# Kernel tuning notes

Hardware: AMD Instinct MI355X
Metric: run time of the kernel (lower is better)

The kernel has to match this reference:

```python
import jax, jax.numpy as jnp
import numpy as np

EMB = 768
HEADS = 8
B, N = 8, 1024

def _ln(x, g, b, eps=1e-5):
    mu = jnp.mean(x, axis=-1, keepdims=True)
    var = jnp.mean(jnp.square(x - mu), axis=-1, keepdims=True)
    return (x - mu) * jax.lax.rsqrt(var + eps) * g + b

def setup_inputs() -> dict:
    key = jax.random.key(0)
    ks = jax.random.split(key, 8)
    s_in = 0.02
    return {
        "x": jax.random.normal(ks[0], (B, N, EMB), jnp.float32),
        "w_qkvr": jax.random.normal(ks[1], (EMB, 4 * EMB), jnp.float32) * s_in,
        "b_qkvr": jnp.zeros((4 * EMB,), jnp.float32),
        "w_proj": jax.random.normal(ks[2], (EMB, EMB), jnp.float32) * s_in,
        "b_proj": jnp.zeros((EMB,), jnp.float32),
        "ln1_g": jnp.ones((EMB,), jnp.float32),
        "ln1_b": jnp.zeros((EMB,), jnp.float32),
        "w_ff1": jax.random.normal(ks[3], (EMB, 4 * EMB), jnp.float32) * s_in,
        "b_ff1": jnp.zeros((4 * EMB,), jnp.float32),
        "w_ff2": jax.random.normal(ks[4], (4 * EMB, EMB), jnp.float32) * s_in,
        "b_ff2": jnp.zeros((EMB,), jnp.float32),
        "ln2_g": jnp.ones((EMB,), jnp.float32),
        "ln2_b": jnp.zeros((EMB,), jnp.float32),
    }

def reference(x, w_qkvr, b_qkvr, w_proj, b_proj, ln1_g, ln1_b,
              w_ff1, b_ff1, w_ff2, b_ff2, ln2_g, ln2_b):
    b, n, e = x.shape
    h = HEADS
    d = e // h
    # fused QKV+R projection; einops '(h d qkvr)' => qkvr is the INNERMOST factor
    qkvr = (x @ w_qkvr + b_qkvr).reshape(b, n, h, d, 4)
    qkvr = jnp.transpose(qkvr, (4, 0, 2, 1, 3))  # [4, b, h, n, d]
    q, k, v, r = qkvr[0], qkvr[1], qkvr[2], qkvr[3]
    energy = jnp.einsum('bhqd,bhkd->bhqk', q, k)
    # quirk: softmax of UNSCALED logits, then divide by sqrt(emb_size) AFTER
    att = jax.nn.softmax(energy, axis=-1) / jnp.sqrt(jnp.float32(e))
    out = jnp.einsum('bhqk,bhkd->bhqd', att, v)
    out = out * r  # elementwise r-gate
    out = jnp.transpose(out, (0, 2, 1, 3)).reshape(b, n, e)
    out = out @ w_proj + b_proj
    x1 = _ln(out + x, ln1_g, ln1_b)  # residual then post-LayerNorm
    ff = jax.nn.gelu(x1 @ w_ff1 + b_ff1, approximate=False) @ w_ff2 + b_ff2
    return _ln(ff + x1, ln2_g, ln2_b)
```

## Files before the change

kernel.cpp:

```cpp
#include <hip/hip_runtime.h>
#include <math.h>


typedef __bf16 bf16_t;
typedef __bf16 bf16x4 __attribute__((ext_vector_type(4)));
typedef __bf16 bf16x8 __attribute__((ext_vector_type(8)));
typedef float f32x4 __attribute__((ext_vector_type(4)));

#define EMB   768
#define HEADS 8
#define DHEAD 96
#define BATCH 8
#define SEQ   1024
#define ROWS  (BATCH * SEQ)

__device__ __forceinline__ void load16_lds(const bf16_t* g, bf16_t* l) {
    __builtin_amdgcn_global_load_lds(
        (__attribute__((address_space(1))) unsigned int*)g,
        (__attribute__((address_space(3))) unsigned int*)l,
        16, 0, 0);
}


__global__ void cvt_bf16_kernel(const float* __restrict__ in, bf16_t* __restrict__ out, int n) {
    int stride = gridDim.x * blockDim.x;
    for (int i = blockIdx.x * blockDim.x + threadIdx.x; i < n; i += stride)
        out[i] = (bf16_t)in[i];
}

__global__ void transpose_cvt_kernel(const float* __restrict__ in, bf16_t* __restrict__ out,
                                     int K, int N) {
    __shared__ float t[32][33];
    int n0 = blockIdx.x * 32, k0 = blockIdx.y * 32;
    int tx = threadIdx.x, ty0 = threadIdx.y;
#pragma unroll
    for (int i = 0; i < 4; i++) {
        int ty = ty0 + 8 * i;
        t[ty][tx] = in[(size_t)(k0 + ty) * N + n0 + tx];
    }
    __syncthreads();
#pragma unroll
    for (int i = 0; i < 4; i++) {
        int ty = ty0 + 8 * i;
        out[(size_t)(n0 + ty) * K + k0 + tx] = (bf16_t)t[tx][ty];
    }
}

__global__ void qkvr_transpose_kernel(const float* __restrict__ in, bf16_t* __restrict__ out) {
    __shared__ float t[32][33];
    int n0 = blockIdx.x * 32, k0 = blockIdx.y * 32;
    int tx = threadIdx.x, ty0 = threadIdx.y;
    const int which = n0 / 768, hd0 = n0 % 768;
#pragma unroll
    for (int i = 0; i < 4; i++) {
        int ty = ty0 + 8 * i;
        t[ty][tx] = in[(size_t)(k0 + ty) * 3072 + (hd0 + tx) * 4 + which];
    }
    __syncthreads();
#pragma unroll
    for (int i = 0; i < 4; i++) {
        int ty = ty0 + 8 * i;
        out[(size_t)(n0 + ty) * 768 + k0 + tx] = (bf16_t)t[tx][ty];
    }
}


enum { EPI_QKVR = 0, EPI_PROJ = 1, EPI_GELU = 2, EPI_FF2 = 3 };

template <int EPI, int KDIM>
__global__ __launch_bounds__(256) void gemm_kernel(
    const bf16_t* __restrict__ A,
    const bf16_t* __restrict__ BT,
    const float* __restrict__ bias,
    bf16_t* __restrict__ qo, bf16_t* __restrict__ ko,
    bf16_t* __restrict__ vTo, bf16_t* __restrict__ ro,
    const float* __restrict__ resid,
    float* __restrict__ outf,
    bf16_t* __restrict__ outb)
{
    __shared__ __align__(16) bf16_t As[128 * 64];
    __shared__ __align__(16) bf16_t Bs[128 * 64];

    const int tid  = threadIdx.x;
    const int wave = tid >> 6, lane = tid & 63;
    const int quad = lane >> 4, col16 = lane & 15;
    const int id = blockIdx.x;
    const int bx = id >> 6;
    const int by = ((id & 7) << 3) | ((id >> 3) & 7);
    const int m0 = by * 128, n0 = bx * 128;
    const int wrow = (wave >> 1) * 64, wcol = (wave & 1) * 64;

    f32x4 acc[4][4] = {};

    size_t ga[4], gb[4];
#pragma unroll
    for (int i = 0; i < 4; i++) {
        const int u = tid + 256 * i;
        const int rr = u >> 3, j = (u & 7) ^ (rr & 7);
        ga[i] = (size_t)(m0 + rr) * KDIM + j * 8;
        gb[i] = (size_t)(n0 + rr) * KDIM + j * 8;
    }

    for (int kk = 0; kk < KDIM / 64; kk++) {
        const int k0 = kk * 64;
        __syncthreads();
#pragma unroll
        for (int i = 0; i < 4; i++) {
            load16_lds(A + ga[i] + k0, As + (tid + 256 * i) * 8);
            load16_lds(BT + gb[i] + k0, Bs + (tid + 256 * i) * 8);
        }
        __syncthreads();
#pragma unroll
        for (int kc = 0; kc < 2; kc++) {
            bf16x8 af[4], bfr[4];
#pragma unroll
            for (int t = 0; t < 4; t++) {
                const int R = wrow + t * 16 + col16;
                af[t] = *reinterpret_cast<const bf16x8*>(As + R * 64 + (((kc * 4 + quad) ^ (R & 7)) * 8));
            }
#pragma unroll
            for (int t = 0; t < 4; t++) {
                const int R = wcol + t * 16 + col16;
                bfr[t] = *reinterpret_cast<const bf16x8*>(Bs + R * 64 + (((kc * 4 + quad) ^ (R & 7)) * 8));
            }
#pragma unroll
            for (int tr = 0; tr < 4; tr++)
#pragma unroll
                for (int tc = 0; tc < 4; tc++)
                    acc[tr][tc] = __builtin_amdgcn_mfma_f32_16x16x32_bf16(af[tr], bfr[tc], acc[tr][tc], 0, 0, 0);
        }
    }

    if (EPI == EPI_QKVR) {
        const int whichb = bx / 6;
        if (whichb == 2) {
#pragma unroll
            for (int tr = 0; tr < 4; tr++) {
#pragma unroll
                for (int tc = 0; tc < 4; tc++) {
                    const int hd   = (bx % 6) * 128 + wcol + tc * 16 + col16;
                    const int head = hd / DHEAD, dd = hd % DHEAD;
                    const float bv = bias[hd * 4 + 2];
                    const int row0 = m0 + wrow + tr * 16 + quad * 4;
                    const int b = row0 >> 10, nn0 = row0 & 1023;
                    bf16x4 w;
#pragma unroll
                    for (int rg = 0; rg < 4; rg++) w[rg] = (bf16_t)(acc[tr][tc][rg] + bv);
                    *reinterpret_cast<bf16x4*>(
                        vTo + ((size_t)(b * HEADS + head) * DHEAD + dd) * SEQ + nn0) = w;
                }
            }
        } else {
            bf16_t* dst = (whichb == 0) ? qo : (whichb == 1) ? ko : ro;
#pragma unroll
            for (int tr = 0; tr < 4; tr++) {
#pragma unroll
                for (int tc = 0; tc < 4; tc++) {
                    const int hd   = (bx % 6) * 128 + wcol + tc * 16 + col16;
                    const int head = hd / DHEAD, dd = hd % DHEAD;
                    const float bv = bias[hd * 4 + whichb];
#pragma unroll
                    for (int rg = 0; rg < 4; rg++) {
                        const int row = m0 + wrow + tr * 16 + quad * 4 + rg;
                        const int b = row >> 10, nn = row & 1023;
                        dst[((size_t)(b * HEADS + head) * SEQ + nn) * DHEAD + dd] =
                            (bf16_t)(acc[tr][tc][rg] + bv);
                    }
                }
            }
        }
    } else {
#pragma unroll
        for (int tr = 0; tr < 4; tr++) {
#pragma unroll
            for (int tc = 0; tc < 4; tc++) {
#pragma unroll
                for (int rg = 0; rg < 4; rg++) {
                    const int row  = m0 + wrow + tr * 16 + quad * 4 + rg;
                    const int colg = n0 + wcol + tc * 16 + col16;
                    float v = acc[tr][tc][rg] + bias[colg];
                    if (EPI == EPI_PROJ || EPI == EPI_FF2) {
                        outf[(size_t)row * EMB + colg] = v + resid[(size_t)row * EMB + colg];
                    } else {
                        const float z = 1.5957691216057308f * v * (1.0f + 0.044715f * v * v);
                        const float g = v / (1.0f + __expf(-z));
                        outb[(size_t)row * 3072 + colg] = (bf16_t)g;
                    }
                }
            }
        }
    }
}


__global__ __launch_bounds__(256) void attn_kernel(
    const bf16_t* __restrict__ q, const bf16_t* __restrict__ k,
    const bf16_t* __restrict__ vT, const bf16_t* __restrict__ r,
    bf16_t* __restrict__ attn_out)
{
    __shared__ __align__(16) bf16_t Ks[64 * 96];
    __shared__ __align__(16) bf16_t Vs[96 * 64];
    __shared__ __align__(16) bf16_t P[4][16 * 72];

    const int tid = threadIdx.x, wave = tid >> 6, lane = tid & 63;
    const int quad = lane >> 4, col = lane & 15;
    const int bh = blockIdx.x & 63, qb = blockIdx.x >> 6;
    const int n0 = qb * 64 + wave * 16;
    const bf16_t* qp = q  + (size_t)bh * SEQ * DHEAD;
    const bf16_t* kb = k  + (size_t)bh * SEQ * DHEAD;
    const bf16_t* vb = vT + (size_t)bh * DHEAD * SEQ;
    bf16_t* Pw = P[wave];

    bf16x8 qf[3];
#pragma unroll
    for (int ks = 0; ks < 3; ks++)
        qf[ks] = *reinterpret_cast<const bf16x8*>(qp + (size_t)(n0 + col) * DHEAD + ks * 32 + quad * 8);

    const int u0 = tid, u1 = tid + 256, u2 = tid + 512;
    const int vf0 = u0 >> 3, vp0 = (u0 & 7) ^ (vf0 & 7);
    const int vf1 = u1 >> 3, vp1 = (u1 & 7) ^ (vf1 & 7);
    const int vf2 = u2 >> 3, vp2 = (u2 & 7) ^ (vf2 & 7);

    f32x4 O[6] = {};
    float lsum = 0.f;

    for (int ch = 0; ch < SEQ / 64; ch++) {
        const int kc0 = ch * 64;
        __syncthreads();
        const bf16_t* ksrc = kb + (size_t)kc0 * DHEAD;
        load16_lds(ksrc + u0 * 8, Ks + u0 * 8);
        load16_lds(ksrc + u1 * 8, Ks + u1 * 8);
        load16_lds(ksrc + u2 * 8, Ks + u2 * 8);
        load16_lds(vb + (size_t)vf0 * SEQ + kc0 + vp0 * 8, Vs + u0 * 8);
        load16_lds(vb + (size_t)vf1 * SEQ + kc0 + vp1 * 8, Vs + u1 * 8);
        load16_lds(vb + (size_t)vf2 * SEQ + kc0 + vp2 * 8, Vs + u2 * 8);
        __syncthreads();

        f32x4 s[4] = {};
#pragma unroll
        for (int ks = 0; ks < 3; ks++) {
#pragma unroll
            for (int h = 0; h < 4; h++) {
                bf16x8 kf = *reinterpret_cast<const bf16x8*>(Ks + (h * 16 + col) * DHEAD + ks * 32 + quad * 8);
                s[h] = __builtin_amdgcn_mfma_f32_16x16x32_bf16(kf, qf[ks], s[h], 0, 0, 0);
            }
        }
#pragma unroll
        for (int h = 0; h < 4; h++) {
            bf16x4 w;
#pragma unroll
            for (int rg = 0; rg < 4; rg++) {
                const float e = __expf(s[h][rg]);
                lsum += e;
                w[rg] = (bf16_t)e;
            }
            *reinterpret_cast<bf16x4*>(Pw + col * 72 + h * 16 + quad * 4) = w;
        }
        bf16x8 af0 = *reinterpret_cast<const bf16x8*>(Pw + col * 72 + quad * 8);
        bf16x8 af1 = *reinterpret_cast<const bf16x8*>(Pw + col * 72 + 32 + quad * 8);
#pragma unroll
        for (int tc = 0; tc < 6; tc++) {
            const int feat = tc * 16 + col;
            bf16x8 bv0 = *reinterpret_cast<const bf16x8*>(Vs + feat * 64 + ((quad)     ^ (col & 7)) * 8);
            bf16x8 bv1 = *reinterpret_cast<const bf16x8*>(Vs + feat * 64 + ((4 + quad) ^ (col & 7)) * 8);
            O[tc] = __builtin_amdgcn_mfma_f32_16x16x32_bf16(af0, bv0, O[tc], 0, 0, 0);
            O[tc] = __builtin_amdgcn_mfma_f32_16x16x32_bf16(af1, bv1, O[tc], 0, 0, 0);
        }
    }

    lsum += __shfl_xor(lsum, 16);
    lsum += __shfl_xor(lsum, 32);

    const float inv_sqrt_emb = 0.036084391824351615f;
    const int b = bh >> 3, h = bh & 7;
#pragma unroll
    for (int rg = 0; rg < 4; rg++) {
        const int nrow = quad * 4 + rg;
        const float lr = __shfl(lsum, nrow);
        const float scale = inv_sqrt_emb / lr;
        const int n = n0 + nrow;
#pragma unroll
        for (int tc = 0; tc < 6; tc++) {
            const int feat = tc * 16 + col;
            const float rv = (float)r[((size_t)bh * SEQ + n) * DHEAD + feat];
            attn_out[((size_t)(b * SEQ + n)) * EMB + h * DHEAD + feat] = (bf16_t)(O[tc][rg] * scale * rv);
        }
    }
}


__global__ __launch_bounds__(256) void ln_kernel(
    const float* __restrict__ in, const float* __restrict__ g, const float* __restrict__ b,
    float* __restrict__ y, bf16_t* __restrict__ yb)
{
    const int row = blockIdx.x * 4 + (threadIdx.x >> 6);
    const int lane = threadIdx.x & 63;
    const float* rp = in + (size_t)row * EMB;
    float v[12];
    float sum = 0.f;
#pragma unroll
    for (int i = 0; i < 12; i++) { v[i] = rp[lane + i * 64]; sum += v[i]; }
#pragma unroll
    for (int off = 32; off; off >>= 1) sum += __shfl_xor(sum, off);
    const float mean = sum * (1.0f / 768.0f);
    float s2 = 0.f;
#pragma unroll
    for (int i = 0; i < 12; i++) { float d = v[i] - mean; s2 += d * d; }
#pragma unroll
    for (int off = 32; off; off >>= 1) s2 += __shfl_xor(s2, off);
    const float inv = rsqrtf(s2 * (1.0f / 768.0f) + 1e-5f);
#pragma unroll
    for (int i = 0; i < 12; i++) {
        const int c = lane + i * 64;
        const float o = (v[i] - mean) * inv * g[c] + b[c];
        y[(size_t)row * EMB + c] = o;
        if (yb) yb[(size_t)row * EMB + c] = (bf16_t)o;
    }
}


extern "C" void kernel_launch(void* const* d_in, const int* in_sizes, int n_in,
                              void* d_out, int out_size, void* d_ws, size_t ws_size,
                              hipStream_t stream)
{
    const float* x      = (const float*)d_in[0];
    const float* w_qkvr = (const float*)d_in[1];
    const float* b_qkvr = (const float*)d_in[2];
    const float* w_proj = (const float*)d_in[3];
    const float* b_proj = (const float*)d_in[4];
    const float* ln1_g  = (const float*)d_in[5];
    const float* ln1_b  = (const float*)d_in[6];
    const float* w_ff1  = (const float*)d_in[7];
    const float* b_ff1  = (const float*)d_in[8];
    const float* w_ff2  = (const float*)d_in[9];
    const float* b_ff2  = (const float*)d_in[10];
    const float* ln2_g  = (const float*)d_in[11];
    const float* ln2_b  = (const float*)d_in[12];
    float* out = (float*)d_out;

    char* ws = (char*)d_ws;
    size_t off = 0;
    auto alloc = [&](size_t bytes) {
        char* p = ws + off;
        off += (bytes + 255) & ~(size_t)255;
        return (void*)p;
    };
    const size_t ACT = (size_t)ROWS * EMB;
    bf16_t* xb      = (bf16_t*)alloc(ACT * 2);
    bf16_t* wqkvrT  = (bf16_t*)alloc((size_t)3072 * 768 * 2);
    bf16_t* wprojT  = (bf16_t*)alloc((size_t)768 * 768 * 2);
    bf16_t* wff1T   = (bf16_t*)alloc((size_t)3072 * 768 * 2);
    bf16_t* wff2T   = (bf16_t*)alloc((size_t)768 * 3072 * 2);
    bf16_t* qbuf    = (bf16_t*)alloc(ACT * 2);
    bf16_t* kbuf    = (bf16_t*)alloc(ACT * 2);
    bf16_t* vTbuf   = (bf16_t*)alloc(ACT * 2);
    bf16_t* rbuf    = (bf16_t*)alloc(ACT * 2);
    bf16_t* attn_o  = (bf16_t*)alloc(ACT * 2);
    float*  x1f     = (float*)alloc(ACT * 4);
    bf16_t* x1b     = (bf16_t*)alloc(ACT * 2);
    bf16_t* ff1     = (bf16_t*)alloc((size_t)ROWS * 3072 * 2);
    float*  res     = out;

    dim3 tb32(32, 8);

    cvt_bf16_kernel<<<2048, 256, 0, stream>>>(x, xb, (int)ACT);
    qkvr_transpose_kernel<<<dim3(3072 / 32, 768 / 32), tb32, 0, stream>>>(w_qkvr, wqkvrT);
    transpose_cvt_kernel<<<dim3(768 / 32, 768 / 32), tb32, 0, stream>>>(w_proj, wprojT, 768, 768);
    transpose_cvt_kernel<<<dim3(3072 / 32, 768 / 32), tb32, 0, stream>>>(w_ff1, wff1T, 768, 3072);
    transpose_cvt_kernel<<<dim3(768 / 32, 3072 / 32), tb32, 0, stream>>>(w_ff2, wff2T, 3072, 768);

    gemm_kernel<EPI_QKVR, 768><<<24 * 64, 256, 0, stream>>>(
        xb, wqkvrT, b_qkvr, qbuf, kbuf, vTbuf, rbuf, nullptr, nullptr, nullptr);

    attn_kernel<<<dim3(SEQ / 64 * BATCH * HEADS), 256, 0, stream>>>(qbuf, kbuf, vTbuf, rbuf, attn_o);

    gemm_kernel<EPI_PROJ, 768><<<6 * 64, 256, 0, stream>>>(
        attn_o, wprojT, b_proj, nullptr, nullptr, nullptr, nullptr, x, res, nullptr);
    ln_kernel<<<2048, 256, 0, stream>>>(res, ln1_g, ln1_b, x1f, x1b);

    gemm_kernel<EPI_GELU, 768><<<24 * 64, 256, 0, stream>>>(
        x1b, wff1T, b_ff1, nullptr, nullptr, nullptr, nullptr, nullptr, nullptr, ff1);

    gemm_kernel<EPI_FF2, 3072><<<6 * 64, 256, 0, stream>>>(
        ff1, wff2T, b_ff2, nullptr, nullptr, nullptr, nullptr, x1f, res, nullptr);
    ln_kernel<<<2048, 256, 0, stream>>>(res, ln2_g, ln2_b, out, nullptr);

    (void)in_sizes; (void)n_in; (void)out_size; (void)ws_size;
}
```

Baseline: 388.8 us.

## Rewrite GEMMs as 8-wave 256x128 tiles with triple-buffered async LDS prefetch

Replaces the 4-wave 128x128 GEMM with an 8-wave, 512-thread kernel that computes 256x128 output tiles. The K loop now uses three LDS buffers, prefetching two K-tiles ahead with split staging, vmcnt waits and raw barriers, plus s_setprio around the MFMA block. Block IDs are remapped across XCDs for locality. The aim is to hide global-load latency behind MFMA work and halve B reloads per output, at the cost of more LDS (144KB per block) and fewer blocks for the small-N GEMMs.

Result: no change. 381.7 us (-1.8%).

```diff
diff --git a/kernel.cpp b/kernel.cpp
--- a/kernel.cpp
+++ b/kernel.cpp
@@ -67,8 +67,8 @@
 
 enum { EPI_QKVR = 0, EPI_PROJ = 1, EPI_GELU = 2, EPI_FF2 = 3 };
 
-template <int EPI, int KDIM>
-__global__ __launch_bounds__(256) void gemm_kernel(
+template <int EPI, int KDIM, int NBX>
+__global__ __launch_bounds__(512, 2) void gemm8p_kernel(
     const bf16_t* __restrict__ A,
     const bf16_t* __restrict__ BT,
     const float* __restrict__ bias,
@@ -78,58 +78,106 @@
     float* __restrict__ outf,
     bf16_t* __restrict__ outb)
 {
-    __shared__ __align__(16) bf16_t As[128 * 64];
-    __shared__ __align__(16) bf16_t Bs[128 * 64];
+    constexpr int NKT  = KDIM / 64;
+    constexpr int BUFE = 24576;
+
+    __shared__ __align__(16) bf16_t lds[3 * BUFE];
 
     const int tid  = threadIdx.x;
     const int wave = tid >> 6, lane = tid & 63;
     const int quad = lane >> 4, col16 = lane & 15;
-    const int id = blockIdx.x;
-    const int bx = id >> 6;
-    const int by = ((id & 7) << 3) | ((id >> 3) & 7);
-    const int m0 = by * 128, n0 = bx * 128;
-    const int wrow = (wave >> 1) * 64, wcol = (wave & 1) * 64;
+    const int wm = wave >> 1, wn = wave & 1;
+
+    const int cpx  = gridDim.x >> 3;
+    const int id   = blockIdx.x;
+    const int wgid = (id & 7) * cpx + (id >> 3);
+    const int bx = wgid % NBX, by = wgid / NBX;
+    const int m0 = by * 256, n0 = bx * 128;
+
+    size_t gA[4]; int lA[4];
+    size_t gB[2]; int lB[2];
+#pragma unroll
+    for (int i = 0; i < 4; i++) {
+        const int u = tid + 512 * i;
+        const int r = u >> 3, j = (u & 7) ^ (r & 7);
+        gA[i] = (size_t)(m0 + r) * KDIM + j * 8;
+        lA[i] = u * 8;
+    }
+#pragma unroll
+    for (int i = 0; i < 2; i++) {
+        const int u = tid + 512 * i;
+        const int r = u >> 3, j = (u & 7) ^ (r & 7);
+        gB[i] = (size_t)(n0 + r) * KDIM + j * 8;
+        lB[i] = 16384 + u * 8;
+    }
+
+#define STAGE_H0(g_, buf_) do { \
+        const int k0_ = (g_) * 64; \
+        load16_lds(A  + gA[0] + k0_, lds + (buf_) * BUFE + lA[0]); \
+        load16_lds(A  + gA[1] + k0_, lds + (buf_) * BUFE + lA[1]); \
+        load16_lds(BT + gB[0] + k0_, lds + (buf_) * BUFE + lB[0]); \
+    } while (0)
+#define STAGE_H1(g_, buf_) do { \
+        const int k0_ = (g_) * 64; \
+        load16_lds(A  + gA[2] + k0_, lds + (buf_) * BUFE + lA[2]); \
+        load16_lds(A  + gA[3] + k0_, lds + (buf_) * BUFE + lA[3]); \
+        load16_lds(BT + gB[1] + k0_, lds + (buf_) * BUFE + lB[1]); \
+    } while (0)
+
+    STAGE_H0(0, 0); STAGE_H1(0, 0);
+    STAGE_H0(1, 1); STAGE_H1(1, 1);
+    asm volatile("s_waitcnt vmcnt(6)" ::: "memory");
+    __builtin_amdgcn_s_barrier();
 
     f32x4 acc[4][4] = {};
 
-    size_t ga[4], gb[4];
-#pragma unroll
-    for (int i = 0; i < 4; i++) {
-        const int u = tid + 256 * i;
-        const int rr = u >> 3, j = (u & 7) ^ (rr & 7);
-        ga[i] = (size_t)(m0 + rr) * KDIM + j * 8;
-        gb[i] = (size_t)(n0 + rr) * KDIM + j * 8;
-    }
-
-    for (int kk = 0; kk < KDIM / 64; kk++) {
-        const int k0 = kk * 64;
-        __syncthreads();
-#pragma unroll
-        for (int i = 0; i < 4; i++) {
-            load16_lds(A + ga[i] + k0, As + (tid + 256 * i) * 8);
-            load16_lds(BT + gb[i] + k0, Bs + (tid + 256 * i) * 8);
-        }
-        __syncthreads();
+#pragma unroll 3
+    for (int g = 0; g < NKT; g++) {
+        const int buf  = g % 3;
+        const int sbuf = (g + 2) % 3;
+        const bf16_t* Ab = lds + buf * BUFE;
+        const bf16_t* Bb = Ab + 16384;
+        const bool do_stage = (g + 2 < NKT);
 #pragma unroll
         for (int kc = 0; kc < 2; kc++) {
             bf16x8 af[4], bfr[4];
 #pragma unroll
             for (int t = 0; t < 4; t++) {
-                const int R = wrow + t * 16 + col16;
-                af[t] = *reinterpret_cast<const bf16x8*>(As + R * 64 + (((kc * 4 + quad) ^ (R & 7)) * 8));
+                const int R = wm * 64 + t * 16 + col16;
+                af[t] = *reinterpret_cast<const bf16x8*>(
+                    Ab + R * 64 + (((kc * 4 + quad) ^ (R & 7)) * 8));
             }
 #pragma unroll
             for (int t = 0; t < 4; t++) {
-                const int R = wcol + t * 16 + col16;
-                bfr[t] = *reinterpret_cast<const bf16x8*>(Bs + R * 64 + (((kc * 4 + quad) ^ (R & 7)) * 8));
-            }
+                const int S = wn * 64 + t * 16 + col16;
+                bfr[t] = *reinterpret_cast<const bf16x8*>(
+                    Bb + S * 64 + (((kc * 4 + quad) ^ (S & 7)) * 8));
+            }
+            if (kc == 0) {
+                if (do_stage) STAGE_H0(g + 2, sbuf);
+            } else {
+                if (do_stage) {
+                    STAGE_H1(g + 2, sbuf);
+                    asm volatile("s_waitcnt vmcnt(6)" ::: "memory");
+                } else if (g + 2 == NKT) {
+                    asm volatile("s_waitcnt vmcnt(0)" ::: "memory");
+                }
+            }
+            __builtin_amdgcn_s_barrier();
+            __builtin_amdgcn_s_setprio(1);
 #pragma unroll
             for (int tr = 0; tr < 4; tr++)
 #pragma unroll
                 for (int tc = 0; tc < 4; tc++)
-                    acc[tr][tc] = __builtin_amdgcn_mfma_f32_16x16x32_bf16(af[tr], bfr[tc], acc[tr][tc], 0, 0, 0);
-        }
-    }
+                    acc[tr][tc] = __builtin_amdgcn_mfma_f32_16x16x32_bf16(
+                        af[tr], bfr[tc], acc[tr][tc], 0, 0, 0);
+            __builtin_amdgcn_s_setprio(0);
+            __builtin_amdgcn_sched_barrier(0);
+            __builtin_amdgcn_s_barrier();
+        }
+    }
+#undef STAGE_H0
+#undef STAGE_H1
 
     if (EPI == EPI_QKVR) {
         const int whichb = bx / 6;
@@ -138,10 +186,10 @@
             for (int tr = 0; tr < 4; tr++) {
 #pragma unroll
                 for (int tc = 0; tc < 4; tc++) {
-                    const int hd   = (bx % 6) * 128 + wcol + tc * 16 + col16;
+                    const int hd   = (bx % 6) * 128 + wn * 64 + tc * 16 + col16;
                     const int head = hd / DHEAD, dd = hd % DHEAD;
                     const float bv = bias[hd * 4 + 2];
-                    const int row0 = m0 + wrow + tr * 16 + quad * 4;
+                    const int row0 = m0 + wm * 64 + tr * 16 + quad * 4;
                     const int b = row0 >> 10, nn0 = row0 & 1023;
                     bf16x4 w;
 #pragma unroll
@@ -156,12 +204,12 @@
             for (int tr = 0; tr < 4; tr++) {
 #pragma unroll
                 for (int tc = 0; tc < 4; tc++) {
-                    const int hd   = (bx % 6) * 128 + wcol + tc * 16 + col16;
+                    const int hd   = (bx % 6) * 128 + wn * 64 + tc * 16 + col16;
                     const int head = hd / DHEAD, dd = hd % DHEAD;
                     const float bv = bias[hd * 4 + whichb];
 #pragma unroll
                     for (int rg = 0; rg < 4; rg++) {
-                        const int row = m0 + wrow + tr * 16 + quad * 4 + rg;
+                        const int row = m0 + wm * 64 + tr * 16 + quad * 4 + rg;
                         const int b = row >> 10, nn = row & 1023;
                         dst[((size_t)(b * HEADS + head) * SEQ + nn) * DHEAD + dd] =
                             (bf16_t)(acc[tr][tc][rg] + bv);
@@ -176,8 +224,8 @@
             for (int tc = 0; tc < 4; tc++) {
 #pragma unroll
                 for (int rg = 0; rg < 4; rg++) {
-                    const int row  = m0 + wrow + tr * 16 + quad * 4 + rg;
-                    const int colg = n0 + wcol + tc * 16 + col16;
+                    const int row  = m0 + wm * 64 + tr * 16 + quad * 4 + rg;
+                    const int colg = n0 + wn * 64 + tc * 16 + col16;
                     float v = acc[tr][tc][rg] + bias[colg];
                     if (EPI == EPI_PROJ || EPI == EPI_FF2) {
                         outf[(size_t)row * EMB + colg] = v + resid[(size_t)row * EMB + colg];
@@ -369,19 +417,19 @@
     transpose_cvt_kernel<<<dim3(3072 / 32, 768 / 32), tb32, 0, stream>>>(w_ff1, wff1T, 768, 3072);
     transpose_cvt_kernel<<<dim3(768 / 32, 3072 / 32), tb32, 0, stream>>>(w_ff2, wff2T, 3072, 768);
 
-    gemm_kernel<EPI_QKVR, 768><<<24 * 64, 256, 0, stream>>>(
+    gemm8p_kernel<EPI_QKVR, 768, 24><<<768, 512, 0, stream>>>(
         xb, wqkvrT, b_qkvr, qbuf, kbuf, vTbuf, rbuf, nullptr, nullptr, nullptr);
 
     attn_kernel<<<dim3(SEQ / 64 * BATCH * HEADS), 256, 0, stream>>>(qbuf, kbuf, vTbuf, rbuf, attn_o);
 
-    gemm_kernel<EPI_PROJ, 768><<<6 * 64, 256, 0, stream>>>(
+    gemm8p_kernel<EPI_PROJ, 768, 6><<<192, 512, 0, stream>>>(
         attn_o, wprojT, b_proj, nullptr, nullptr, nullptr, nullptr, x, res, nullptr);
     ln_kernel<<<2048, 256, 0, stream>>>(res, ln1_g, ln1_b, x1f, x1b);
 
-    gemm_kernel<EPI_GELU, 768><<<24 * 64, 256, 0, stream>>>(
+    gemm8p_kernel<EPI_GELU, 768, 24><<<768, 512, 0, stream>>>(
         x1b, wff1T, b_ff1, nullptr, nullptr, nullptr, nullptr, nullptr, nullptr, ff1);
 
-    gemm_kernel<EPI_FF2, 3072><<<6 * 64, 256, 0, stream>>>(
+    gemm8p_kernel<EPI_FF2, 3072, 6><<<192, 512, 0, stream>>>(
         ff1, wff2T, b_ff2, nullptr, nullptr, nullptr, nullptr, x1f, res, nullptr);
     ln_kernel<<<2048, 256, 0, stream>>>(res, ln2_g, ln2_b, out, nullptr);
 
```

## Replace 128x128 GEMM with 256x256 double-buffered 8-wave kernel and split-K FF2

Applied to the files above, without the earlier changes.

Swaps every GEMM for a 256x256-tile, 512-thread kernel. It double-buffers its LDS and issues loads asynchronously a quarter-tile ahead, with explicit vmcnt waits, barriers and raised priority around the MFMA blocks. The FF2 GEMM is split along K into two halves: the second half writes raw partial sums into the reused q buffer, and the second LayerNorm adds them in. Larger tiles and overlapped loads aim to raise operand reuse and MFMA utilisation. The trade-offs are fewer workgroups for the proj GEMM (96 blocks), heavy register pressure, and an extra fp32 partial buffer to write and read.

After: 423.7 us. +9.0%, slower.

```diff
diff --git a/kernel.cpp b/kernel.cpp
--- a/kernel.cpp
+++ b/kernel.cpp
@@ -67,8 +67,81 @@
 
 enum { EPI_QKVR = 0, EPI_PROJ = 1, EPI_GELU = 2, EPI_FF2 = 3 };
 
-template <int EPI, int KDIM>
-__global__ __launch_bounds__(256) void gemm_kernel(
+#define VMW6 asm volatile("s_waitcnt vmcnt(6)" ::: "memory")
+#define VMW0 asm volatile("s_waitcnt vmcnt(0)" ::: "memory")
+
+#define READ_A(MH, ABUF) do { \
+    _Pragma("unroll") for (int mi = 0; mi < 4; mi++) { \
+        const int R_ = (MH) * 128 + wm * 64 + mi * 16 + col16; \
+        _Pragma("unroll") for (int kc = 0; kc < 2; kc++) { \
+            af[mi][kc] = *reinterpret_cast<const bf16x8*>( \
+                (ABUF) + R_ * 64 + (((kc * 4 + quad) ^ (R_ & 7)) * 8)); \
+        } \
+    } \
+} while (0)
+
+#define READ_B(NH, BBUF) do { \
+    _Pragma("unroll") for (int ni = 0; ni < 2; ni++) { \
+        const int S_ = (NH) * 128 + wn * 32 + ni * 16 + col16; \
+        _Pragma("unroll") for (int kc = 0; kc < 2; kc++) { \
+            bfr[ni][kc] = *reinterpret_cast<const bf16x8*>( \
+                (BBUF) + S_ * 64 + (((kc * 4 + quad) ^ (S_ & 7)) * 8)); \
+        } \
+    } \
+} while (0)
+
+#define MFMAS(MH, NH) do { \
+    __builtin_amdgcn_s_setprio(1); \
+    _Pragma("unroll") for (int mi = 0; mi < 4; mi++) { \
+        _Pragma("unroll") for (int ni = 0; ni < 2; ni++) { \
+            _Pragma("unroll") for (int kc = 0; kc < 2; kc++) { \
+                acc[MH][mi][NH][ni] = __builtin_amdgcn_mfma_f32_16x16x32_bf16( \
+                    af[mi][kc], bfr[ni][kc], acc[MH][mi][NH][ni], 0, 0, 0); \
+            } \
+        } \
+    } \
+    __builtin_amdgcn_s_setprio(0); \
+    __builtin_amdgcn_sched_barrier(0); \
+} while (0)
+
+#define STAGE(h_, t_, pd_) do { \
+    bf16_t* db_ = lds + (pd_) * 32768; \
+    const bf16_t* sp_ = ((h_) < 2 ? A : BT); \
+    load16_lds(sp_ + gof[h_][0] + (size_t)(t_) * 64, db_ + lof[h_][0]); \
+    load16_lds(sp_ + gof[h_][1] + (size_t)(t_) * 64, db_ + lof[h_][1]); \
+} while (0)
+
+#define TILE4(t_, PAR, S1, S234, VM) do { \
+    const bf16_t* Ab_ = lds + (PAR) * 32768; \
+    const bf16_t* Bb_ = Ab_ + 16384; \
+     \
+    READ_A(0, Ab_); READ_B(0, Bb_); \
+    if (S1) STAGE(2, (t_) + 1, (PAR) ^ 1); \
+    VM; __builtin_amdgcn_s_barrier(); \
+    MFMAS(0, 0); \
+    __builtin_amdgcn_s_barrier(); \
+     \
+    READ_B(1, Bb_); \
+    if (S234) STAGE(0, (t_) + 2, PAR); \
+    VM; __builtin_amdgcn_s_barrier(); \
+    MFMAS(0, 1); \
+    __builtin_amdgcn_s_barrier(); \
+     \
+    READ_A(1, Ab_); \
+    if (S234) STAGE(3, (t_) + 2, PAR); \
+    VM; __builtin_amdgcn_s_barrier(); \
+    MFMAS(1, 1); \
+    __builtin_amdgcn_s_barrier(); \
+     \
+    READ_B(0, Bb_); \
+    if (S234) STAGE(1, (t_) + 2, PAR); \
+    VM; __builtin_amdgcn_s_barrier(); \
+    MFMAS(1, 0); \
+    __builtin_amdgcn_s_barrier(); \
+} while (0)
+
+template <int EPI, int KSTRIDE, int NKT, int NBX, int SPLIT>
+__global__ __launch_bounds__(512, 2) void gemm256_kernel(
     const bf16_t* __restrict__ A,
     const bf16_t* __restrict__ BT,
     const float* __restrict__ bias,
@@ -76,116 +149,127 @@
     bf16_t* __restrict__ vTo, bf16_t* __restrict__ ro,
     const float* __restrict__ resid,
     float* __restrict__ outf,
-    bf16_t* __restrict__ outb)
+    bf16_t* __restrict__ outb,
+    float* __restrict__ outf2)
 {
-    __shared__ __align__(16) bf16_t As[128 * 64];
-    __shared__ __align__(16) bf16_t Bs[128 * 64];
+    __shared__ __align__(16) bf16_t lds[2 * 32768];
 
     const int tid  = threadIdx.x;
     const int wave = tid >> 6, lane = tid & 63;
     const int quad = lane >> 4, col16 = lane & 15;
-    const int id = blockIdx.x;
-    const int bx = id >> 6;
-    const int by = ((id & 7) << 3) | ((id >> 3) & 7);
-    const int m0 = by * 128, n0 = bx * 128;
-    const int wrow = (wave >> 1) * 64, wcol = (wave & 1) * 64;
-
-    f32x4 acc[4][4] = {};
-
-    size_t ga[4], gb[4];
-#pragma unroll
-    for (int i = 0; i < 4; i++) {
-        const int u = tid + 256 * i;
-        const int rr = u >> 3, j = (u & 7) ^ (rr & 7);
-        ga[i] = (size_t)(m0 + rr) * KDIM + j * 8;
-        gb[i] = (size_t)(n0 + rr) * KDIM + j * 8;
-    }
-
-    for (int kk = 0; kk < KDIM / 64; kk++) {
-        const int k0 = kk * 64;
-        __syncthreads();
-#pragma unroll
-        for (int i = 0; i < 4; i++) {
-            load16_lds(A + ga[i] + k0, As + (tid + 256 * i) * 8);
-            load16_lds(BT + gb[i] + k0, Bs + (tid + 256 * i) * 8);
-        }
-        __syncthreads();
-#pragma unroll
-        for (int kc = 0; kc < 2; kc++) {
-            bf16x8 af[4], bfr[4];
-#pragma unroll
-            for (int t = 0; t < 4; t++) {
-                const int R = wrow + t * 16 + col16;
-                af[t] = *reinterpret_cast<const bf16x8*>(As + R * 64 + (((kc * 4 + quad) ^ (R & 7)) * 8));
-            }
-#pragma unroll
-            for (int t = 0; t < 4; t++) {
-                const int R = wcol + t * 16 + col16;
-                bfr[t] = *reinterpret_cast<const bf16x8*>(Bs + R * 64 + (((kc * 4 + quad) ^ (R & 7)) * 8));
-            }
-#pragma unroll
-            for (int tr = 0; tr < 4; tr++)
-#pragma unroll
-                for (int tc = 0; tc < 4; tc++)
-                    acc[tr][tc] = __builtin_amdgcn_mfma_f32_16x16x32_bf16(af[tr], bfr[tc], acc[tr][tc], 0, 0, 0);
-        }
-    }
+    const int wm = wave >> 2, wn = wave & 3;
+
+    const int cpx  = gridDim.x >> 3;
+    const int id   = blockIdx.x;
+    const int wgid = (id & 7) * cpx + (id >> 3);
+    int byy = wgid / NBX;
+    int split = 0;
+    if (SPLIT) { split = byy >> 5; byy &= 31; }
+    const int bx = wgid % NBX, by = byy;
+    const int m0 = by * 256, n0 = bx * 256;
+    if (SPLIT) { A += (size_t)split * (NKT * 64); BT += (size_t)split * (NKT * 64); }
+
+    size_t gof[4][2];
+    int    lof[4][2];
+#pragma unroll
+    for (int i = 0; i < 2; i++) {
+        const int u = tid + i * 512;
+        const int r = u >> 3;
+        const int j = (u & 7) ^ (r & 7);
+#pragma unroll
+        for (int h = 0; h < 2; h++) {
+            gof[h][i]     = (size_t)(m0 + h * 128 + r) * KSTRIDE + j * 8;
+            gof[2 + h][i] = (size_t)(n0 + h * 128 + r) * KSTRIDE + j * 8;
+            lof[h][i]     = (h * 1024 + u) * 8;
+            lof[2 + h][i] = 16384 + (h * 1024 + u) * 8;
+        }
+    }
+
+    f32x4 acc[2][4][2][2] = {};
+    bf16x8 af[4][2], bfr[2][2];
+
+    STAGE(0, 0, 0); STAGE(3, 0, 0); STAGE(1, 0, 0); STAGE(2, 0, 0);
+    STAGE(0, 1, 1); STAGE(3, 1, 1); STAGE(1, 1, 1);
+    VMW6; __builtin_amdgcn_s_barrier();
+
+    for (int tt = 0; tt < NKT / 2 - 1; ++tt) {
+        const int t0 = 2 * tt;
+        TILE4(t0,     0, 1, 1, VMW6);
+        TILE4(t0 + 1, 1, 1, 1, VMW6);
+    }
+    TILE4(NKT - 2, 0, 1, 0, VMW0);
+    TILE4(NKT - 1, 1, 0, 0, VMW0);
 
     if (EPI == EPI_QKVR) {
-        const int whichb = bx / 6;
+        const int whichb = bx / 3;
+        const int hdbase = (bx % 3) * 256;
         if (whichb == 2) {
 #pragma unroll
-            for (int tr = 0; tr < 4; tr++) {
-#pragma unroll
-                for (int tc = 0; tc < 4; tc++) {
-                    const int hd   = (bx % 6) * 128 + wcol + tc * 16 + col16;
-                    const int head = hd / DHEAD, dd = hd % DHEAD;
-                    const float bv = bias[hd * 4 + 2];
-                    const int row0 = m0 + wrow + tr * 16 + quad * 4;
-                    const int b = row0 >> 10, nn0 = row0 & 1023;
-                    bf16x4 w;
-#pragma unroll
-                    for (int rg = 0; rg < 4; rg++) w[rg] = (bf16_t)(acc[tr][tc][rg] + bv);
-                    *reinterpret_cast<bf16x4*>(
-                        vTo + ((size_t)(b * HEADS + head) * DHEAD + dd) * SEQ + nn0) = w;
-                }
+            for (int mh = 0; mh < 2; mh++)
+#pragma unroll
+            for (int mi = 0; mi < 4; mi++)
+#pragma unroll
+            for (int nh = 0; nh < 2; nh++)
+#pragma unroll
+            for (int ni = 0; ni < 2; ni++) {
+                const int hd   = hdbase + nh * 128 + wn * 32 + ni * 16 + col16;
+                const int head = hd / DHEAD, dd = hd % DHEAD;
+                const float bv = bias[hd * 4 + 2];
+                const int row0 = m0 + mh * 128 + wm * 64 + mi * 16 + quad * 4;
+                const int b = row0 >> 10, nn0 = row0 & 1023;
+                bf16x4 w;
+#pragma unroll
+                for (int rg = 0; rg < 4; rg++) w[rg] = (bf16_t)(acc[mh][mi][nh][ni][rg] + bv);
+                *reinterpret_cast<bf16x4*>(
+                    vTo + ((size_t)(b * HEADS + head) * DHEAD + dd) * SEQ + nn0) = w;
             }
         } else {
             bf16_t* dst = (whichb == 0) ? qo : (whichb == 1) ? ko : ro;
 #pragma unroll
-            for (int tr = 0; tr < 4; tr++) {
-#pragma unroll
-                for (int tc = 0; tc < 4; tc++) {
-                    const int hd   = (bx % 6) * 128 + wcol + tc * 16 + col16;
-                    const int head = hd / DHEAD, dd = hd % DHEAD;
-                    const float bv = bias[hd * 4 + whichb];
-#pragma unroll
-                    for (int rg = 0; rg < 4; rg++) {
-                        const int row = m0 + wrow + tr * 16 + quad * 4 + rg;
-                        const int b = row >> 10, nn = row & 1023;
-                        dst[((size_t)(b * HEADS + head) * SEQ + nn) * DHEAD + dd] =
-                            (bf16_t)(acc[tr][tc][rg] + bv);
-                    }
+            for (int mh = 0; mh < 2; mh++)
+#pragma unroll
+            for (int mi = 0; mi < 4; mi++)
+#pragma unroll
+            for (int nh = 0; nh < 2; nh++)
+#pragma unroll
+            for (int ni = 0; ni < 2; ni++) {
+                const int hd   = hdbase + nh * 128 + wn * 32 + ni * 16 + col16;
+                const int head = hd / DHEAD, dd = hd % DHEAD;
+                const float bv = bias[hd * 4 + whichb];
+#pragma unroll
+                for (int rg = 0; rg < 4; rg++) {
+                    const int row = m0 + mh * 128 + wm * 64 + mi * 16 + quad * 4 + rg;
+                    const int b = row >> 10, nn = row & 1023;
+                    dst[((size_t)(b * HEADS + head) * SEQ + nn) * DHEAD + dd] =
+                        (bf16_t)(acc[mh][mi][nh][ni][rg] + bv);
                 }
             }
         }
     } else {
-#pragma unroll
-        for (int tr = 0; tr < 4; tr++) {
-#pragma unroll
-            for (int tc = 0; tc < 4; tc++) {
-#pragma unroll
-                for (int rg = 0; rg < 4; rg++) {
-                    const int row  = m0 + wrow + tr * 16 + quad * 4 + rg;
-                    const int colg = n0 + wcol + tc * 16 + col16;
-                    float v = acc[tr][tc][rg] + bias[colg];
-                    if (EPI == EPI_PROJ || EPI == EPI_FF2) {
-                        outf[(size_t)row * EMB + colg] = v + resid[(size_t)row * EMB + colg];
-                    } else {
-                        const float z = 1.5957691216057308f * v * (1.0f + 0.044715f * v * v);
-                        const float g = v / (1.0f + __expf(-z));
-                        outb[(size_t)row * 3072 + colg] = (bf16_t)g;
-                    }
+        const bool part = (SPLIT != 0) && (split == 1);
+#pragma unroll
+        for (int mh = 0; mh < 2; mh++)
+#pragma unroll
+        for (int mi = 0; mi < 4; mi++)
+#pragma unroll
+        for (int nh = 0; nh < 2; nh++)
+#pragma unroll
+        for (int ni = 0; ni < 2; ni++) {
+            const int colg = n0 + nh * 128 + wn * 32 + ni * 16 + col16;
+#pragma unroll
+            for (int rg = 0; rg < 4; rg++) {
+                const int row = m0 + mh * 128 + wm * 64 + mi * 16 + quad * 4 + rg;
+                const float a = acc[mh][mi][nh][ni][rg];
+                if (EPI == EPI_GELU) {
+                    const float v = a + bias[colg];
+                    const float z = 1.5957691216057308f * v * (1.0f + 0.044715f * v * v);
+                    const float g = v / (1.0f + __expf(-z));
+                    outb[(size_t)row * 3072 + colg] = (bf16_t)g;
+                } else if (part) {
+                    outf2[(size_t)row * EMB + colg] = a;
+                } else {
+                    outf[(size_t)row * EMB + colg] =
+                        a + bias[colg] + resid[(size_t)row * EMB + colg];
                 }
             }
         }
@@ -290,16 +374,22 @@
 
 
 __global__ __launch_bounds__(256) void ln_kernel(
-    const float* __restrict__ in, const float* __restrict__ g, const float* __restrict__ b,
+    const float* __restrict__ in, const float* __restrict__ in2,
+    const float* __restrict__ g, const float* __restrict__ b,
     float* __restrict__ y, bf16_t* __restrict__ yb)
 {
     const int row = blockIdx.x * 4 + (threadIdx.x >> 6);
     const int lane = threadIdx.x & 63;
     const float* rp = in + (size_t)row * EMB;
+    const float* rp2 = in2 ? in2 + (size_t)row * EMB : nullptr;
     float v[12];
     float sum = 0.f;
 #pragma unroll
-    for (int i = 0; i < 12; i++) { v[i] = rp[lane + i * 64]; sum += v[i]; }
+    for (int i = 0; i < 12; i++) {
+        v[i] = rp[lane + i * 64];
+        if (in2) v[i] += rp2[lane + i * 64];
+        sum += v[i];
+    }
 #pragma unroll
     for (int off = 32; off; off >>= 1) sum += __shfl_xor(sum, off);
     const float mean = sum * (1.0f / 768.0f);
@@ -360,6 +450,7 @@
     bf16_t* x1b     = (bf16_t*)alloc(ACT * 2);
     bf16_t* ff1     = (bf16_t*)alloc((size_t)ROWS * 3072 * 2);
     float*  res     = out;
+    float*  res2    = (float*)qbuf;
 
     dim3 tb32(32, 8);
 
@@ -369,21 +460,21 @@
     transpose_cvt_kernel<<<dim3(3072 / 32, 768 / 32), tb32, 0, stream>>>(w_ff1, wff1T, 768, 3072);
     transpose_cvt_kernel<<<dim3(768 / 32, 3072 / 32), tb32, 0, stream>>>(w_ff2, wff2T, 3072, 768);
 
-    gemm_kernel<EPI_QKVR, 768><<<24 * 64, 256, 0, stream>>>(
-        xb, wqkvrT, b_qkvr, qbuf, kbuf, vTbuf, rbuf, nullptr, nullptr, nullptr);
+    gemm256_kernel<EPI_QKVR, 768, 12, 12, 0><<<384, 512, 0, stream>>>(
+        xb, wqkvrT, b_qkvr, qbuf, kbuf, vTbuf, rbuf, nullptr, nullptr, nullptr, nullptr);
 
     attn_kernel<<<dim3(SEQ / 64 * BATCH * HEADS), 256, 0, stream>>>(qbuf, kbuf, vTbuf, rbuf, attn_o);
 
-    gemm_kernel<EPI_PROJ, 768><<<6 * 64, 256, 0, stream>>>(
-        attn_o, wprojT, b_proj, nullptr, nullptr, nullptr, nullptr, x, res, nullptr);
-    ln_kernel<<<2048, 256, 0, stream>>>(res, ln1_g, ln1_b, x1f, x1b);
-
-    gemm_kernel<EPI_GELU, 768><<<24 * 64, 256, 0, stream>>>(
-        x1b, wff1T, b_ff1, nullptr, nullptr, nullptr, nullptr, nullptr, nullptr, ff1);
-
-    gemm_kernel<EPI_FF2, 3072><<<6 * 64, 256, 0, stream>>>(
-        ff1, wff2T, b_ff2, nullptr, nullptr, nullptr, nullptr, x1f, res, nullptr);
-    ln_kernel<<<2048, 256, 0, stream>>>(res, ln2_g, ln2_b, out, nullptr);
+    gemm256_kernel<EPI_PROJ, 768, 12, 3, 0><<<96, 512, 0, stream>>>(
+        attn_o, wprojT, b_proj, nullptr, nullptr, nullptr, nullptr, x, res, nullptr, nullptr);
+    ln_kernel<<<2048, 256, 0, stream>>>(res, nullptr, ln1_g, ln1_b, x1f, x1b);
+
+    gemm256_kernel<EPI_GELU, 768, 12, 12, 0><<<384, 512, 0, stream>>>(
+        x1b, wff1T, b_ff1, nullptr, nullptr, nullptr, nullptr, nullptr, nullptr, ff1, nullptr);
+
+    gemm256_kernel<EPI_FF2, 3072, 24, 3, 1><<<192, 512, 0, stream>>>(
+        ff1, wff2T, b_ff2, nullptr, nullptr, nullptr, nullptr, x1f, res, nullptr, res2);
+    ln_kernel<<<2048, 256, 0, stream>>>(res, res2, ln2_g, ln2_b, out, nullptr);
 
     (void)in_sizes; (void)n_in; (void)out_size; (void)ws_size;
 }
```

## Rewrite GEMMs as triple-buffered 256x128 tiles with 512 threads

Applied to the files above, without the earlier changes.

Replaces the single-buffered 128x128 GEMM with a 512-thread kernel that computes 256x128 output tiles, sharing each B tile across two wave groups. It uses a three-stage LDS ring with global_load_lds prefetch two tiles ahead, vmcnt-based waits and raised MFMA priority, so memory loads overlap with compute and fewer barriers are needed. Block-to-tile mapping is changed to an XCD-aware swizzle. The larger LDS footprint (144 KB) may reduce occupancy, and the epilogue keeps the 128-row wave layout, so correctness depends on the epilogue handling m0 with 256-row tiles.

Result: no change. 384.5 us (-1.1%).

```diff
diff --git a/kernel.cpp b/kernel.cpp
--- a/kernel.cpp
+++ b/kernel.cpp
@@ -67,8 +67,46 @@
 
 enum { EPI_QKVR = 0, EPI_PROJ = 1, EPI_GELU = 2, EPI_FF2 = 3 };
 
-template <int EPI, int KDIM>
-__global__ __launch_bounds__(256) void gemm_kernel(
+#define VMW6 asm volatile("s_waitcnt vmcnt(6)" ::: "memory")
+#define VMW0 asm volatile("s_waitcnt vmcnt(0)" ::: "memory")
+#define VMNONE do {} while (0)
+
+#define RD8(KC, LB) do { \
+    _Pragma("unroll") for (int u = 0; u < 4; u++) { \
+        af[u]  = *reinterpret_cast<const bf16x8*>((LB) + aoff[KC][u]); \
+        bfr[u] = *reinterpret_cast<const bf16x8*>((LB) + boff[KC][u]); \
+    } \
+} while (0)
+
+#define MM16() do { \
+    __builtin_amdgcn_s_setprio(1); \
+    _Pragma("unroll") for (int tr = 0; tr < 4; tr++) \
+        _Pragma("unroll") for (int tc = 0; tc < 4; tc++) \
+            acc[tr][tc] = __builtin_amdgcn_mfma_f32_16x16x32_bf16( \
+                af[tr], bfr[tc], acc[tr][tc], 0, 0, 0); \
+    __builtin_amdgcn_s_setprio(0); \
+} while (0)
+
+#define STAGE6(DB) do { \
+    bf16_t* db_ = lds + (DB) * 24576; \
+    _Pragma("unroll") for (int i2 = 0; i2 < 4; i2++) { load16_lds(pa[i2], db_ + lA[i2]); pa[i2] += 64; } \
+    _Pragma("unroll") for (int i2 = 0; i2 < 2; i2++) { load16_lds(pb[i2], db_ + lB[i2]); pb[i2] += 64; } \
+} while (0)
+
+#define TILE1(BUF, DOSTAGE, GATE, DOBAR) do { \
+    const char* lb_ = (const char*)lds + (BUF) * 49152; \
+    bf16x8 af[4], bfr[4]; \
+    RD8(0, lb_); \
+    if (DOSTAGE) STAGE6(((BUF) + 2) % 3); \
+    MM16(); \
+    RD8(1, lb_); \
+    MM16(); \
+    GATE; \
+    if (DOBAR) { __builtin_amdgcn_sched_barrier(0); __builtin_amdgcn_s_barrier(); } \
+} while (0)
+
+template <int EPI, int KSTRIDE, int NKT, int NBX>
+__global__ __launch_bounds__(512, 2) void gemmsb_kernel(
     const bf16_t* __restrict__ A,
     const bf16_t* __restrict__ BT,
     const float* __restrict__ bias,
@@ -78,58 +116,62 @@
     float* __restrict__ outf,
     bf16_t* __restrict__ outb)
 {
-    __shared__ __align__(16) bf16_t As[128 * 64];
-    __shared__ __align__(16) bf16_t Bs[128 * 64];
+    __shared__ __align__(16) bf16_t lds[3 * 24576];
 
     const int tid  = threadIdx.x;
     const int wave = tid >> 6, lane = tid & 63;
     const int quad = lane >> 4, col16 = lane & 15;
-    const int id = blockIdx.x;
-    const int bx = id >> 6;
-    const int by = ((id & 7) << 3) | ((id >> 3) & 7);
-    const int m0 = by * 128, n0 = bx * 128;
     const int wrow = (wave >> 1) * 64, wcol = (wave & 1) * 64;
 
+    const int cpx  = gridDim.x >> 3;
+    const int id   = blockIdx.x;
+    const int wgid = (id & 7) * cpx + (id >> 3);
+    const int bx = wgid % NBX, by = wgid / NBX;
+    const int m0 = by * 256, n0 = bx * 128;
+
+    int aoff[2][4], boff[2][4];
+#pragma unroll
+    for (int kc = 0; kc < 2; kc++) {
+#pragma unroll
+        for (int u = 0; u < 4; u++) {
+            const int R = wrow + u * 16 + col16;
+            aoff[kc][u] = R * 128 + (((kc * 4 + quad) ^ (R & 7)) * 16);
+            const int S = wcol + u * 16 + col16;
+            boff[kc][u] = 32768 + S * 128 + (((kc * 4 + quad) ^ (S & 7)) * 16);
+        }
+    }
+
+    const bf16_t* pa[4]; const bf16_t* pb[2];
+    int lA[4], lB[2];
+#pragma unroll
+    for (int i = 0; i < 4; i++) {
+        const int u = tid + 512 * i;
+        const int r = u >> 3, j = (u & 7) ^ (r & 7);
+        pa[i] = A + (size_t)(m0 + r) * KSTRIDE + j * 8;
+        lA[i] = u * 8;
+    }
+#pragma unroll
+    for (int i = 0; i < 2; i++) {
+        const int u = tid + 512 * i;
+        const int r = u >> 3, j = (u & 7) ^ (r & 7);
+        pb[i] = BT + (size_t)(n0 + r) * KSTRIDE + j * 8;
+        lB[i] = 16384 + u * 8;
+    }
+
     f32x4 acc[4][4] = {};
 
-    size_t ga[4], gb[4];
-#pragma unroll
-    for (int i = 0; i < 4; i++) {
-        const int u = tid + 256 * i;
-        const int rr = u >> 3, j = (u & 7) ^ (rr & 7);
-        ga[i] = (size_t)(m0 + rr) * KDIM + j * 8;
-        gb[i] = (size_t)(n0 + rr) * KDIM + j * 8;
-    }
-
-    for (int kk = 0; kk < KDIM / 64; kk++) {
-        const int k0 = kk * 64;
-        __syncthreads();
-#pragma unroll
-        for (int i = 0; i < 4; i++) {
-            load16_lds(A + ga[i] + k0, As + (tid + 256 * i) * 8);
-            load16_lds(BT + gb[i] + k0, Bs + (tid + 256 * i) * 8);
-        }
-        __syncthreads();
-#pragma unroll
-        for (int kc = 0; kc < 2; kc++) {
-            bf16x8 af[4], bfr[4];
-#pragma unroll
-            for (int t = 0; t < 4; t++) {
-                const int R = wrow + t * 16 + col16;
-                af[t] = *reinterpret_cast<const bf16x8*>(As + R * 64 + (((kc * 4 + quad) ^ (R & 7)) * 8));
-            }
-#pragma unroll
-            for (int t = 0; t < 4; t++) {
-                const int R = wcol + t * 16 + col16;
-                bfr[t] = *reinterpret_cast<const bf16x8*>(Bs + R * 64 + (((kc * 4 + quad) ^ (R & 7)) * 8));
-            }
-#pragma unroll
-            for (int tr = 0; tr < 4; tr++)
-#pragma unroll
-                for (int tc = 0; tc < 4; tc++)
-                    acc[tr][tc] = __builtin_amdgcn_mfma_f32_16x16x32_bf16(af[tr], bfr[tc], acc[tr][tc], 0, 0, 0);
-        }
-    }
+    STAGE6(0); STAGE6(1);
+    VMW6; __builtin_amdgcn_s_barrier();
+
+#pragma unroll 1
+    for (int tg = 0; tg < NKT / 3 - 1; ++tg) {
+        TILE1(0, 1, VMW6, 1);
+        TILE1(1, 1, VMW6, 1);
+        TILE1(2, 1, VMW6, 1);
+    }
+    TILE1(0, 1, VMW6, 1);
+    TILE1(1, 0, VMW0, 1);
+    TILE1(2, 0, VMNONE, 0);
 
     if (EPI == EPI_QKVR) {
         const int whichb = bx / 6;
@@ -369,19 +411,19 @@
     transpose_cvt_kernel<<<dim3(3072 / 32, 768 / 32), tb32, 0, stream>>>(w_ff1, wff1T, 768, 3072);
     transpose_cvt_kernel<<<dim3(768 / 32, 3072 / 32), tb32, 0, stream>>>(w_ff2, wff2T, 3072, 768);
 
-    gemm_kernel<EPI_QKVR, 768><<<24 * 64, 256, 0, stream>>>(
+    gemmsb_kernel<EPI_QKVR, 768, 12, 24><<<768, 512, 0, stream>>>(
         xb, wqkvrT, b_qkvr, qbuf, kbuf, vTbuf, rbuf, nullptr, nullptr, nullptr);
 
     attn_kernel<<<dim3(SEQ / 64 * BATCH * HEADS), 256, 0, stream>>>(qbuf, kbuf, vTbuf, rbuf, attn_o);
 
-    gemm_kernel<EPI_PROJ, 768><<<6 * 64, 256, 0, stream>>>(
+    gemmsb_kernel<EPI_PROJ, 768, 12, 6><<<192, 512, 0, stream>>>(
         attn_o, wprojT, b_proj, nullptr, nullptr, nullptr, nullptr, x, res, nullptr);
     ln_kernel<<<2048, 256, 0, stream>>>(res, ln1_g, ln1_b, x1f, x1b);
 
-    gemm_kernel<EPI_GELU, 768><<<24 * 64, 256, 0, stream>>>(
+    gemmsb_kernel<EPI_GELU, 768, 12, 24><<<768, 512, 0, stream>>>(
         x1b, wff1T, b_ff1, nullptr, nullptr, nullptr, nullptr, nullptr, nullptr, ff1);
 
-    gemm_kernel<EPI_FF2, 3072><<<6 * 64, 256, 0, stream>>>(
+    gemmsb_kernel<EPI_FF2, 3072, 48, 6><<<192, 512, 0, stream>>>(
         ff1, wff2T, b_ff2, nullptr, nullptr, nullptr, nullptr, x1f, res, nullptr);
     ln_kernel<<<2048, 256, 0, stream>>>(res, ln2_g, ln2_b, out, nullptr);
 
```
